# Performance work log

Measured on AMD Instinct MI355X. Metric: run time of the kernel, lower is better.

## Reference

```python
import jax, jax.numpy as jnp
import numpy as np
import math

B, T, C = 4, 1024, 768
H, K = 12, 10
D = C // H  # 64


def setup_inputs() -> dict:
    key = jax.random.key(0)
    ks = jax.random.split(key, 8)
    s = 1.0 / math.sqrt(C)
    return {
        "hidden_states": jax.random.normal(ks[0], (B, T, C), jnp.float32),
        "ucb_count_score": jax.random.uniform(ks[1], (B, H, T, T), jnp.float32),
        "Wq": jax.random.normal(ks[2], (C, C), jnp.float32) * s,
        "bq": jnp.zeros((C,), jnp.float32),
        "Wk": jax.random.normal(ks[3], (C, C), jnp.float32) * s,
        "bk": jnp.zeros((C,), jnp.float32),
        "Wv": jax.random.normal(ks[4], (C, C), jnp.float32) * s,
        "bv": jnp.zeros((C,), jnp.float32),
        "Wo": jax.random.normal(ks[5], (C, C), jnp.float32) * s,
        "bo": jnp.zeros((C,), jnp.float32),
        "counter": 2000,
        "ucb": 1,
    }


def _heads(x):
    # [B,T,C] -> [B,H,T,D]
    return x.reshape(B, T, H, D).transpose(0, 2, 1, 3)


def reference(hidden_states, ucb_count_score, Wq, bq, Wk, bk, Wv, bv, Wo, bo, counter, ucb):
    q = _heads(hidden_states @ Wq + bq)
    k = _heads(hidden_states @ Wk + bk)
    v = _heads(hidden_states @ Wv + bv)

    scores = jnp.einsum("bhqd,bhkd->bhqk", q, k) / math.sqrt(D)
    att = jax.nn.softmax(scores, axis=-1)

    if ucb and counter >= 1000:  # ucb_activation_step
        log_t = math.log(float(counter))
        ucb_scores = att + 1.0 * jnp.sqrt(log_t / (ucb_count_score + 1e-8))  # ucb_beta=1.0
        _, top_idx = jax.lax.top_k(ucb_scores, K)  # [B,H,T,K]
        # scatter 1.0 at top-k positions along last axis
        flat_idx = top_idx.reshape(-1, K)            # [N,K], N=B*H*T
        n = flat_idx.shape[0]
        mask = jnp.zeros((n, T), att.dtype).at[jnp.arange(n)[:, None], flat_idx].set(1.0)
        mask = mask.reshape(B, H, T, T)
        updated_count = ucb_count_score + mask
        sel = att * mask
        attention_probs = sel / (sel.sum(axis=-1, keepdims=True) + 1e-8)
    else:
        attention_probs = att
        updated_count = ucb_count_score

    ctx = jnp.einsum("bhqk,bhkd->bhqd", attention_probs, v)
    ctx = ctx.transpose(0, 2, 1, 3).reshape(B, T, C)
    out = ctx @ Wo + bo  # proj_dropout is identity in eval
    return out, attention_probs, updated_count
```

## Files before the change

### kernel.cpp

```cpp
#include <hip/hip_runtime.h>
#include <math.h>

namespace {

constexpr int Bc = 4, Tc = 1024, Cch = 768, Hc = 12, Dc = 64, KSEL = 10;
constexpr size_t BTC    = (size_t)Bc * Tc * Cch;
constexpr size_t PROBSN = (size_t)Bc * Hc * Tc * Tc;
constexpr size_t CC     = (size_t)Cch * Cch;

typedef __attribute__((ext_vector_type(8))) short          bf16x8;
typedef __attribute__((ext_vector_type(4))) float          f32x4;
typedef __attribute__((ext_vector_type(8))) unsigned short u16x8;

__device__ __forceinline__ unsigned short bf16rne(float x) {
  unsigned int u = __float_as_uint(x);
  return (unsigned short)((u + 0x7FFFu + ((u >> 16) & 1u)) >> 16);
}
__device__ __forceinline__ float bf16tof(unsigned short h) {
  return __uint_as_float(((unsigned int)h) << 16);
}

__device__ __forceinline__ void split8(const float4 v0, const float4 v1,
                                       u16x8& hh, u16x8& ll) {
  const float xs[8] = {v0.x, v0.y, v0.z, v0.w, v1.x, v1.y, v1.z, v1.w};
  #pragma unroll
  for (int e = 0; e < 8; ++e) {
    const unsigned short hb = bf16rne(xs[e]);
    hh[e] = hb;
    ll[e] = bf16rne(xs[e] - bf16tof(hb));
  }
}

template <int CTRL, int RM, bool BC>
__device__ __forceinline__ float dppmovf(float x, float oldv) {
  return __int_as_float(__builtin_amdgcn_update_dpp(
      __float_as_int(oldv), __float_as_int(x), CTRL, RM, 0xf, BC));
}

__device__ __forceinline__ float wave_fmax(float x) {
  x = fmaxf(x, dppmovf<0x111, 0xf, false>(x, x));
  x = fmaxf(x, dppmovf<0x112, 0xf, false>(x, x));
  x = fmaxf(x, dppmovf<0x114, 0xf, false>(x, x));
  x = fmaxf(x, dppmovf<0x118, 0xf, false>(x, x));
  x = fmaxf(x, dppmovf<0x142, 0xa, false>(x, x));
  x = fmaxf(x, dppmovf<0x143, 0xc, false>(x, x));
  return __int_as_float(__builtin_amdgcn_readlane(__float_as_int(x), 63));
}

__device__ __forceinline__ float wave_fsum(float x) {
  x += dppmovf<0x111, 0xf, true>(x, 0.f);
  x += dppmovf<0x112, 0xf, true>(x, 0.f);
  x += dppmovf<0x114, 0xf, true>(x, 0.f);
  x += dppmovf<0x118, 0xf, true>(x, 0.f);
  x += dppmovf<0x142, 0xa, true>(x, 0.f);
  x += dppmovf<0x143, 0xc, true>(x, 0.f);
  return __int_as_float(__builtin_amdgcn_readlane(__float_as_int(x), 63));
}

template <int CTRL, int RM>
__device__ __forceinline__ unsigned long long dppmax64_step(unsigned long long k) {
  const int lo = (int)(unsigned)(k & 0xFFFFFFFFull);
  const int hi = (int)(unsigned)(k >> 32);
  const int lo2 = __builtin_amdgcn_update_dpp(lo, lo, CTRL, RM, 0xf, false);
  const int hi2 = __builtin_amdgcn_update_dpp(hi, hi, CTRL, RM, 0xf, false);
  const unsigned long long k2 =
      ((unsigned long long)(unsigned)hi2 << 32) | (unsigned)lo2;
  return (k2 > k) ? k2 : k;
}

__device__ __forceinline__ unsigned long long wave_kmax(unsigned long long k) {
  k = dppmax64_step<0x111, 0xf>(k);
  k = dppmax64_step<0x112, 0xf>(k);
  k = dppmax64_step<0x114, 0xf>(k);
  k = dppmax64_step<0x118, 0xf>(k);
  k = dppmax64_step<0x142, 0xa>(k);
  k = dppmax64_step<0x143, 0xc>(k);
  const int lo = __builtin_amdgcn_readlane((int)(unsigned)(k & 0xFFFFFFFFull), 63);
  const int hi = __builtin_amdgcn_readlane((int)(unsigned)(k >> 32), 63);
  return ((unsigned long long)(unsigned)hi << 32) | (unsigned)lo;
}

__device__ __forceinline__ void splitT_body(
    const float* __restrict__ W,
    unsigned short* __restrict__ th, unsigned short* __restrict__ tl)
{
  __shared__ float tile[32][33];
  const int n0 = blockIdx.x * 32, k0 = blockIdx.y * 32;
  const int x = threadIdx.x & 31, y = threadIdx.x >> 5;

  #pragma unroll
  for (int i = 0; i < 4; ++i) {
    const int kk = y * 4 + i;
    tile[kk][x] = W[(size_t)(k0 + kk) * Cch + n0 + x];
  }
  __syncthreads();
  #pragma unroll
  for (int i = 0; i < 4; ++i) {
    const int nn = y * 4 + i;
    const float v = tile[x][nn];
    const unsigned short hb = bf16rne(v);
    th[(size_t)(n0 + nn) * Cch + k0 + x] = hb;
    tl[(size_t)(n0 + nn) * Cch + k0 + x] = bf16rne(v - bf16tof(hb));
  }
}

__global__ __launch_bounds__(256) void splitT_w(
    const float* __restrict__ W,
    unsigned short* __restrict__ th, unsigned short* __restrict__ tl)
{
  splitT_body(W, th, tl);
}

__global__ __launch_bounds__(256) void splitT_w3(
    const float* __restrict__ W0, const float* __restrict__ W1,
    const float* __restrict__ W2,
    unsigned short* __restrict__ th0, unsigned short* __restrict__ tl0,
    unsigned short* __restrict__ th1, unsigned short* __restrict__ tl1,
    unsigned short* __restrict__ th2, unsigned short* __restrict__ tl2)
{
  const int z = blockIdx.z;
  const float* W = (z == 0) ? W0 : (z == 1) ? W1 : W2;
  unsigned short* th = (z == 0) ? th0 : (z == 1) ? th1 : th2;
  unsigned short* tl = (z == 0) ? tl0 : (z == 1) ? tl1 : tl2;
  splitT_body(W, th, tl);
}

__global__ __launch_bounds__(256) void qkv_mfma(
    const float* __restrict__ hid,
    const unsigned short* __restrict__ wqth, const unsigned short* __restrict__ wqtl,
    const unsigned short* __restrict__ wkth, const unsigned short* __restrict__ wktl,
    const unsigned short* __restrict__ wvth, const unsigned short* __restrict__ wvtl,
    const float* __restrict__ bq, const float* __restrict__ bk,
    const float* __restrict__ bv,
    unsigned short* __restrict__ qh, unsigned short* __restrict__ ql,
    unsigned short* __restrict__ kh, unsigned short* __restrict__ kl,
    float* __restrict__ V)
{
  const int z = blockIdx.z;
  const unsigned short* __restrict__ Bhp = (z == 0) ? wqth : (z == 1) ? wkth : wvth;
  const unsigned short* __restrict__ Blp = (z == 0) ? wqtl : (z == 1) ? wktl : wvtl;
  const float* __restrict__ bias = (z == 0) ? bq : (z == 1) ? bk : bv;

  const int m0 = blockIdx.y * 64;
  const int n0 = blockIdx.x * 128;

  __shared__ unsigned short Ah[64][72],  Al[64][72];
  __shared__ unsigned short Bh[128][72], Bl[128][72];

  const int t    = threadIdx.x;
  const int lane = t & 63;
  const int wv   = t >> 6;
  const int wq   = (wv >> 1) * 32;
  const int wk   = (wv & 1) * 64;
  const int fr   = lane & 15;
  const int fg   = lane >> 4;

  f32x4 acc[2][4] = {};

  for (int k0 = 0; k0 < Cch; k0 += 64) {
    __syncthreads();
    #pragma unroll
    for (int i = 0; i < 2; ++i) {
      const int id = t + 256*i;
      const int r = id >> 3, c8 = (id & 7) * 8;
      const float4 v0 = *(const float4*)&hid[(size_t)(m0 + r)*Cch + k0 + c8];
      const float4 v1 = *(const float4*)&hid[(size_t)(m0 + r)*Cch + k0 + c8 + 4];
      u16x8 hh, ll;
      split8(v0, v1, hh, ll);
      *(u16x8*)&Ah[r][c8] = hh;
      *(u16x8*)&Al[r][c8] = ll;
    }
    #pragma unroll
    for (int i = 0; i < 4; ++i) {
      const int id = t + 256*i;
      const int r = id >> 3, c8 = (id & 7) * 8;
      *(u16x8*)&Bh[r][c8] = *(const u16x8*)&Bhp[(size_t)(n0 + r)*Cch + k0 + c8];
      *(u16x8*)&Bl[r][c8] = *(const u16x8*)&Blp[(size_t)(n0 + r)*Cch + k0 + c8];
    }
    __syncthreads();

    #pragma unroll
    for (int g2 = 0; g2 < 2; ++g2) {
      const int dof = g2*32 + 8*fg;
      bf16x8 aH[2], aL[2];
      #pragma unroll
      for (int qt = 0; qt < 2; ++qt) {
        aH[qt] = *(const bf16x8*)&Ah[wq + qt*16 + fr][dof];
        aL[qt] = *(const bf16x8*)&Al[wq + qt*16 + fr][dof];
      }
      #pragma unroll
      for (int kt = 0; kt < 4; ++kt) {
        const bf16x8 bH = *(const bf16x8*)&Bh[wk + kt*16 + fr][dof];
        const bf16x8 bL = *(const bf16x8*)&Bl[wk + kt*16 + fr][dof];
        #pragma unroll
        for (int qt = 0; qt < 2; ++qt) {
          acc[qt][kt] = __builtin_amdgcn_mfma_f32_16x16x32_bf16(
              aH[qt], bH, acc[qt][kt], 0, 0, 0);
          acc[qt][kt] = __builtin_amdgcn_mfma_f32_16x16x32_bf16(
              aH[qt], bL, acc[qt][kt], 0, 0, 0);
          acc[qt][kt] = __builtin_amdgcn_mfma_f32_16x16x32_bf16(
              aL[qt], bH, acc[qt][kt], 0, 0, 0);
        }
      }
    }
  }

  float bcol[4];
  #pragma unroll
  for (int kt = 0; kt < 4; ++kt) bcol[kt] = bias[n0 + wk + kt*16 + fr];

  unsigned short* __restrict__ dh = (z == 0) ? qh : kh;
  unsigned short* __restrict__ dl = (z == 0) ? ql : kl;

  #pragma unroll
  for (int qt = 0; qt < 2; ++qt) {
    #pragma unroll
    for (int j = 0; j < 4; ++j) {
      const int m  = m0 + wq + qt*16 + 4*fg + j;
      const int b  = m >> 10, tt = m & 1023;
      #pragma unroll
      for (int kt = 0; kt < 4; ++kt) {
        const int col = n0 + wk + kt*16 + fr;
        const float val = acc[qt][kt][j] + bcol[kt];
        const size_t idx =
            (((size_t)(b*Hc + (col >> 6)))*Tc + tt)*Dc + (col & 63);
        if (z < 2) {
          const unsigned short hb = bf16rne(val);
          dh[idx] = hb;
          dl[idx] = bf16rne(val - bf16tof(hb));
        } else {
          V[idx] = val;
        }
      }
    }
  }
}

__global__ __launch_bounds__(256) void score_mfma(
    const unsigned short* __restrict__ qhp, const unsigned short* __restrict__ qlp,
    const unsigned short* __restrict__ khp, const unsigned short* __restrict__ klp,
    float* __restrict__ scores)
{
  const int q0 = blockIdx.x * 64;
  const int bh = blockIdx.y;

  __shared__ unsigned short Qh[64][72],  Ql[64][72];
  __shared__ unsigned short Kh[128][72], Kl[128][72];

  const int t = threadIdx.x;
  const size_t qb = ((size_t)bh*Tc + q0) * Dc;

  #pragma unroll
  for (int i = 0; i < 2; ++i) {
    const int id = t + 256*i;
    const int r = id >> 3, c8 = (id & 7) * 8;
    *(u16x8*)&Qh[r][c8] = *(const u16x8*)&qhp[qb + (size_t)r*Dc + c8];
    *(u16x8*)&Ql[r][c8] = *(const u16x8*)&qlp[qb + (size_t)r*Dc + c8];
  }

  const int lane = t & 63;
  const int wv   = t >> 6;
  const int wq   = (wv >> 1) * 32;
  const int wk   = (wv & 1) * 64;
  const int fr   = lane & 15;
  const int fg   = lane >> 4;

  #pragma unroll 1
  for (int kc = 0; kc < 8; ++kc) {
    const int k0 = kc * 128;
    const size_t kb = ((size_t)bh*Tc + k0) * Dc;
    __syncthreads();
    #pragma unroll
    for (int i = 0; i < 4; ++i) {
      const int id = t + 256*i;
      const int r = id >> 3, c8 = (id & 7) * 8;
      *(u16x8*)&Kh[r][c8] = *(const u16x8*)&khp[kb + (size_t)r*Dc + c8];
      *(u16x8*)&Kl[r][c8] = *(const u16x8*)&klp[kb + (size_t)r*Dc + c8];
    }
    __syncthreads();

    f32x4 acc[2][4] = {};
    #pragma unroll
    for (int g2 = 0; g2 < 2; ++g2) {
      const int dof = g2*32 + 8*fg;
      bf16x8 aH[2], aL[2];
      #pragma unroll
      for (int qt = 0; qt < 2; ++qt) {
        aH[qt] = *(const bf16x8*)&Qh[wq + qt*16 + fr][dof];
        aL[qt] = *(const bf16x8*)&Ql[wq + qt*16 + fr][dof];
      }
      #pragma unroll
      for (int kt = 0; kt < 4; ++kt) {
        const bf16x8 bH = *(const bf16x8*)&Kh[wk + kt*16 + fr][dof];
        const bf16x8 bL = *(const bf16x8*)&Kl[wk + kt*16 + fr][dof];
        #pragma unroll
        for (int qt = 0; qt < 2; ++qt) {
          acc[qt][kt] = __builtin_amdgcn_mfma_f32_16x16x32_bf16(
              aH[qt], bH, acc[qt][kt], 0, 0, 0);
          acc[qt][kt] = __builtin_amdgcn_mfma_f32_16x16x32_bf16(
              aH[qt], bL, acc[qt][kt], 0, 0, 0);
          acc[qt][kt] = __builtin_amdgcn_mfma_f32_16x16x32_bf16(
              aL[qt], bH, acc[qt][kt], 0, 0, 0);
        }
      }
    }

    #pragma unroll
    for (int qt = 0; qt < 2; ++qt) {
      #pragma unroll
      for (int j = 0; j < 4; ++j) {
        const int qrow = q0 + wq + qt*16 + 4*fg + j;
        const size_t rb = ((size_t)bh * Tc + qrow) * Tc + k0 + wk;
        #pragma unroll
        for (int kt = 0; kt < 4; ++kt)
          scores[rb + kt*16 + fr] = acc[qt][kt][j] * 0.125f;
      }
    }
  }
}

__global__ __launch_bounds__(256, 4) void ucb_topk(
    const float* __restrict__ qkv,
    const float* __restrict__ count_in,
    const int*   __restrict__ counter_p,
    const int*   __restrict__ ucb_p,
    float* __restrict__ probs,
    float* __restrict__ count_out,
    float* __restrict__ ctx)
{
  const int bh   = blockIdx.y;
  const int lane = threadIdx.x & 63;
  const int wv   = threadIdx.x >> 6;
  const int row  = blockIdx.x * 4 + wv;
  const int b = bh / Hc, h = bh % Hc;
  const size_t rb = ((size_t)bh * Tc + row) * Tc;
  const float* __restrict__ Vh = qkv + 2*BTC + (size_t)bh * Tc * Dc;

  __shared__ float psel[4][KSEL];

  const int  counter = counter_p[0];
  const int  ucbf    = ucb_p[0];
  const bool do_ucb  = (ucbf != 0) && (counter >= 1000);
  const float lt     = do_ucb ? logf((float)counter) : 0.f;

  float s[16];
  #pragma unroll
  for (int w = 0; w < 16; ++w) s[w] = probs[rb + lane + 64*w];

  float mx = -INFINITY;
  #pragma unroll
  for (int w = 0; w < 16; ++w) mx = fmaxf(mx, s[w]);
  mx = wave_fmax(mx);

  float sum = 0.f;
  #pragma unroll
  for (int w = 0; w < 16; ++w) { s[w] = __expf(s[w] - mx); sum += s[w]; }
  sum = wave_fsum(sum);

  const float rsum = 1.0f / sum;
  #pragma unroll
  for (int w = 0; w < 16; ++w) s[w] = s[w] * rsum;

  if (do_ucb) {
    const float sqlt = sqrtf(lt);

    unsigned long long key[16];
    #pragma unroll
    for (int w = 0; w < 16; ++w) {
      const float c = count_in[rb + lane + 64*w];
      count_out[rb + lane + 64*w] = c;
      const float u = fmaf(sqlt, rsqrtf(c + 1e-8f), s[w]);
      key[w] = ((unsigned long long)__float_as_uint(u) << 32)
             | (unsigned long long)(~(unsigned)(lane + (w << 6)));
    }

    unsigned selmask = 0u;
    unsigned long long rpack = 0ull;
    int ks[KSEL];

    #pragma unroll
    for (int r = 0; r < KSEL; ++r) {
      unsigned long long t0[8];
      #pragma unroll
      for (int w = 0; w < 8; ++w) {
        const unsigned long long a =
            ((selmask >> (2*w)) & 1u) ? 0ull : key[2*w];
        const unsigned long long bb =
            ((selmask >> (2*w + 1)) & 1u) ? 0ull : key[2*w + 1];
        t0[w] = (a > bb) ? a : bb;
      }
      unsigned long long t1[4];
      #pragma unroll
      for (int w = 0; w < 4; ++w)
        t1[w] = (t0[2*w] > t0[2*w+1]) ? t0[2*w] : t0[2*w+1];
      unsigned long long t2a = (t1[0] > t1[1]) ? t1[0] : t1[1];
      unsigned long long t2b = (t1[2] > t1[3]) ? t1[2] : t1[3];
      unsigned long long m   = (t2a > t2b) ? t2a : t2b;

      m = wave_kmax(m);

      const int idx = (int)(~(unsigned)(m & 0xFFFFFFFFull));
      ks[r] = idx;
      if ((idx & 63) == lane) {
        const int wsel = idx >> 6;
        selmask |= 1u << wsel;
        rpack   |= ((unsigned long long)r) << (4 * wsel);
      }
    }

    #pragma unroll
    for (int w = 0; w < 16; ++w) {
      if ((selmask >> w) & 1u) {
        const int r = (int)((rpack >> (4 * w)) & 15ull);
        psel[wv][r] = s[w];
      }
    }
    __syncthreads();

    float pvv[KSEL];
    float denom = 1e-8f;
    #pragma unroll
    for (int r = 0; r < KSEL; ++r) { pvv[r] = psel[wv][r]; denom += pvv[r]; }
    const float rden = 1.0f / denom;

    #pragma unroll
    for (int w = 0; w < 16; ++w) {
      const bool sb = (selmask >> w) & 1u;
      probs[rb + lane + 64*w] = sb ? (s[w] * rden) : 0.0f;
    }
    #pragma unroll
    for (int r = 0; r < KSEL; ++r) {
      if ((ks[r] & 63) == lane)
        count_out[rb + ks[r]] = count_in[rb + ks[r]] + 1.0f;
    }

    float cd = 0.f;
    #pragma unroll
    for (int r = 0; r < KSEL; ++r)
      cd += pvv[r] * Vh[(size_t)ks[r] * Dc + lane];
    ctx[((size_t)b*Tc + row)*Cch + h*Dc + lane] = cd * rden;
  } else {
    #pragma unroll
    for (int w = 0; w < 16; ++w) {
      probs[rb + lane + 64*w]     = s[w];
      count_out[rb + lane + 64*w] = count_in[rb + lane + 64*w];
    }
  }
}

__global__ __launch_bounds__(256) void pv_gemm(
    const float* __restrict__ probs,
    const float* __restrict__ Vm,
    float* __restrict__ ctx,
    const int* __restrict__ counter_p,
    const int* __restrict__ ucb_p)
{
  if ((ucb_p[0] != 0) && (counter_p[0] >= 1000)) return;

  const int bh = blockIdx.y;
  const int q0 = blockIdx.x * 64;
  const int b = bh / Hc, h = bh % Hc;

  __shared__ float aT[32][68];
  __shared__ float vN[32][68];

  const int t  = threadIdx.x;
  const int tn = t & 15;
  const int tq = t >> 4;

  float acc[4][4];
  #pragma unroll
  for (int i = 0; i < 4; ++i)
    #pragma unroll
    for (int j = 0; j < 4; ++j) acc[i][j] = 0.f;

  for (int k0 = 0; k0 < Tc; k0 += 32) {
    __syncthreads();
    #pragma unroll
    for (int p = 0; p < 2; ++p) {
      const int id = t + 256*p;
      const int r = id >> 3, c = id & 7;
      const float4 v =
          *(const float4*)&probs[((size_t)bh*Tc + q0 + r)*Tc + k0 + 4*c];
      aT[4*c + 0][r] = v.x; aT[4*c + 1][r] = v.y;
      aT[4*c + 2][r] = v.z; aT[4*c + 3][r] = v.w;
    }
    #pragma unroll
    for (int p = 0; p < 2; ++p) {
      const int id = t + 256*p;
      const int kk = id >> 4, dcc = id & 15;
      const float4 v = *(const float4*)&Vm[((size_t)bh*Tc + k0 + kk)*Dc + 4*dcc];
      *(float4*)&vN[kk][4*dcc] = v;
    }
    __syncthreads();
    #pragma unroll
    for (int kk = 0; kk < 32; ++kk) {
      const float4 a  = *(const float4*)&aT[kk][4*tq];
      const float4 vv = *(const float4*)&vN[kk][4*tn];
      const float av[4] = {a.x, a.y, a.z, a.w};
      const float bw[4] = {vv.x, vv.y, vv.z, vv.w};
      #pragma unroll
      for (int qi = 0; qi < 4; ++qi)
        #pragma unroll
        for (int ni = 0; ni < 4; ++ni) acc[qi][ni] += av[qi] * bw[ni];
    }
  }

  #pragma unroll
  for (int qi = 0; qi < 4; ++qi) {
    const int tt = q0 + 4*tq + qi;
    float4 o;
    o.x = acc[qi][0]; o.y = acc[qi][1]; o.z = acc[qi][2]; o.w = acc[qi][3];
    *(float4*)&ctx[((size_t)b*Tc + tt)*Cch + h*Dc + 4*tn] = o;
  }
}

__global__ __launch_bounds__(256) void out_mfma(
    const float* __restrict__ ctx,
    const unsigned short* __restrict__ bth, const unsigned short* __restrict__ btl,
    const float* __restrict__ bias,
    float* __restrict__ out)
{
  const int m0 = blockIdx.y * 64;
  const int n0 = blockIdx.x * 128;

  __shared__ unsigned short Ah[64][72],  Al[64][72];
  __shared__ unsigned short Bh[128][72], Bl[128][72];

  const int t    = threadIdx.x;
  const int lane = t & 63;
  const int wv   = t >> 6;
  const int wq   = (wv >> 1) * 32;
  const int wk   = (wv & 1) * 64;
  const int fr   = lane & 15;
  const int fg   = lane >> 4;

  f32x4 acc[2][4] = {};

  for (int k0 = 0; k0 < Cch; k0 += 64) {
    __syncthreads();
    #pragma unroll
    for (int i = 0; i < 2; ++i) {
      const int id = t + 256*i;
      const int r = id >> 3, c8 = (id & 7) * 8;
      const float4 v0 = *(const float4*)&ctx[(size_t)(m0 + r)*Cch + k0 + c8];
      const float4 v1 = *(const float4*)&ctx[(size_t)(m0 + r)*Cch + k0 + c8 + 4];
      u16x8 hh, ll;
      split8(v0, v1, hh, ll);
      *(u16x8*)&Ah[r][c8] = hh;
      *(u16x8*)&Al[r][c8] = ll;
    }
    #pragma unroll
    for (int i = 0; i < 4; ++i) {
      const int id = t + 256*i;
      const int r = id >> 3, c8 = (id & 7) * 8;
      *(u16x8*)&Bh[r][c8] = *(const u16x8*)&bth[(size_t)(n0 + r)*Cch + k0 + c8];
      *(u16x8*)&Bl[r][c8] = *(const u16x8*)&btl[(size_t)(n0 + r)*Cch + k0 + c8];
    }
    __syncthreads();

    #pragma unroll
    for (int g2 = 0; g2 < 2; ++g2) {
      const int dof = g2*32 + 8*fg;
      bf16x8 aH[2], aL[2];
      #pragma unroll
      for (int qt = 0; qt < 2; ++qt) {
        aH[qt] = *(const bf16x8*)&Ah[wq + qt*16 + fr][dof];
        aL[qt] = *(const bf16x8*)&Al[wq + qt*16 + fr][dof];
      }
      #pragma unroll
      for (int kt = 0; kt < 4; ++kt) {
        const bf16x8 bH = *(const bf16x8*)&Bh[wk + kt*16 + fr][dof];
        const bf16x8 bL = *(const bf16x8*)&Bl[wk + kt*16 + fr][dof];
        #pragma unroll
        for (int qt = 0; qt < 2; ++qt) {
          acc[qt][kt] = __builtin_amdgcn_mfma_f32_16x16x32_bf16(
              aH[qt], bH, acc[qt][kt], 0, 0, 0);
          acc[qt][kt] = __builtin_amdgcn_mfma_f32_16x16x32_bf16(
              aH[qt], bL, acc[qt][kt], 0, 0, 0);
          acc[qt][kt] = __builtin_amdgcn_mfma_f32_16x16x32_bf16(
              aL[qt], bH, acc[qt][kt], 0, 0, 0);
        }
      }
    }
  }

  float bcol[4];
  #pragma unroll
  for (int kt = 0; kt < 4; ++kt) bcol[kt] = bias[n0 + wk + kt*16 + fr];

  #pragma unroll
  for (int qt = 0; qt < 2; ++qt) {
    #pragma unroll
    for (int j = 0; j < 4; ++j) {
      const int m = m0 + wq + qt*16 + 4*fg + j;
      #pragma unroll
      for (int kt = 0; kt < 4; ++kt) {
        const int col = n0 + wk + kt*16 + fr;
        out[(size_t)m * Cch + col] = acc[qt][kt][j] + bcol[kt];
      }
    }
  }
}

}

extern "C" void kernel_launch(void* const* d_in, const int* in_sizes, int n_in,
                              void* d_out, int out_size, void* d_ws, size_t ws_size,
                              hipStream_t stream) {
  (void)in_sizes; (void)n_in; (void)out_size; (void)ws_size;

  const float* hid  = (const float*)d_in[0];
  const float* cnt  = (const float*)d_in[1];
  const float* Wq   = (const float*)d_in[2];
  const float* bq   = (const float*)d_in[3];
  const float* Wk   = (const float*)d_in[4];
  const float* bk   = (const float*)d_in[5];
  const float* Wv   = (const float*)d_in[6];
  const float* bv   = (const float*)d_in[7];
  const float* Wo   = (const float*)d_in[8];
  const float* bo   = (const float*)d_in[9];
  const int* counter = (const int*)d_in[10];
  const int* ucb     = (const int*)d_in[11];

  float* out       = (float*)d_out;
  float* probs     = out + BTC;
  float* count_out = probs + PROBSN;

  float* ws  = (float*)d_ws;
  float* V   = ws + 2*BTC;
  float* ctx = ws + 3*BTC;
  unsigned short* qkb = (unsigned short*)d_ws;
  unsigned short* qh = qkb;
  unsigned short* ql = qkb + BTC;
  unsigned short* kh = qkb + 2*BTC;
  unsigned short* kl = qkb + 3*BTC;

  unsigned short* cvt  = (unsigned short*)count_out;
  unsigned short* wqth = cvt;
  unsigned short* wqtl = wqth + CC;
  unsigned short* wkth = wqtl + CC;
  unsigned short* wktl = wkth + CC;
  unsigned short* wvth = wktl + CC;
  unsigned short* wvtl = wvth + CC;

  unsigned short* woth = qkb;
  unsigned short* wotl = qkb + CC;

  splitT_w3<<<dim3(24, 24, 3), 256, 0, stream>>>(
      Wq, Wk, Wv, wqth, wqtl, wkth, wktl, wvth, wvtl);

  qkv_mfma<<<dim3(Cch/128, (Bc*Tc)/64, 3), 256, 0, stream>>>(
      hid, wqth, wqtl, wkth, wktl, wvth, wvtl,
      bq, bk, bv, qh, ql, kh, kl, V);

  score_mfma<<<dim3(Tc/64, Bc*Hc), 256, 0, stream>>>(
      qh, ql, kh, kl, probs);

  splitT_w<<<dim3(24, 24), 256, 0, stream>>>(Wo, woth, wotl);

  ucb_topk<<<dim3(Tc/4, Bc*Hc), 256, 0, stream>>>(
      ws, cnt, counter, ucb, probs, count_out, ctx);

  pv_gemm<<<dim3(Tc/64, Bc*Hc), 256, 0, stream>>>(
      probs, V, ctx, counter, ucb);

  out_mfma<<<dim3(Cch/128, (Bc*Tc)/64), 256, 0, stream>>>(
      ctx, woth, wotl, bo, out);
}
```

Before: 371.6 us.

## Fuse QK score computation into softmax/UCB top-k kernel

Merges the score GEMM and the softmax/UCB top-k kernel. Each 1024-thread block computes QK^T scores for 16 query rows through LDS and keeps them in registers, so the full fp32 score matrix is no longer written to and re-read from global memory. The cost is that every block reloads all of K for only 16 query rows. Each wave also does just one 16x16 MFMA tile per chunk, with a large LDS footprint and lower occupancy.

```diff
diff --git a/kernel.cpp b/kernel.cpp
--- a/kernel.cpp
+++ b/kernel.cpp
@@ -236,90 +236,9 @@
   }
 }
 
-__global__ __launch_bounds__(256) void score_mfma(
+__global__ __launch_bounds__(1024, 4) void score_topk(
     const unsigned short* __restrict__ qhp, const unsigned short* __restrict__ qlp,
     const unsigned short* __restrict__ khp, const unsigned short* __restrict__ klp,
-    float* __restrict__ scores)
-{
-  const int q0 = blockIdx.x * 64;
-  const int bh = blockIdx.y;
-
-  __shared__ unsigned short Qh[64][72],  Ql[64][72];
-  __shared__ unsigned short Kh[128][72], Kl[128][72];
-
-  const int t = threadIdx.x;
-  const size_t qb = ((size_t)bh*Tc + q0) * Dc;
-
-  #pragma unroll
-  for (int i = 0; i < 2; ++i) {
-    const int id = t + 256*i;
-    const int r = id >> 3, c8 = (id & 7) * 8;
-    *(u16x8*)&Qh[r][c8] = *(const u16x8*)&qhp[qb + (size_t)r*Dc + c8];
-    *(u16x8*)&Ql[r][c8] = *(const u16x8*)&qlp[qb + (size_t)r*Dc + c8];
-  }
-
-  const int lane = t & 63;
-  const int wv   = t >> 6;
-  const int wq   = (wv >> 1) * 32;
-  const int wk   = (wv & 1) * 64;
-  const int fr   = lane & 15;
-  const int fg   = lane >> 4;
-
-  #pragma unroll 1
-  for (int kc = 0; kc < 8; ++kc) {
-    const int k0 = kc * 128;
-    const size_t kb = ((size_t)bh*Tc + k0) * Dc;
-    __syncthreads();
-    #pragma unroll
-    for (int i = 0; i < 4; ++i) {
-      const int id = t + 256*i;
-      const int r = id >> 3, c8 = (id & 7) * 8;
-      *(u16x8*)&Kh[r][c8] = *(const u16x8*)&khp[kb + (size_t)r*Dc + c8];
-      *(u16x8*)&Kl[r][c8] = *(const u16x8*)&klp[kb + (size_t)r*Dc + c8];
-    }
-    __syncthreads();
-
-    f32x4 acc[2][4] = {};
-    #pragma unroll
-    for (int g2 = 0; g2 < 2; ++g2) {
-      const int dof = g2*32 + 8*fg;
-      bf16x8 aH[2], aL[2];
-      #pragma unroll
-      for (int qt = 0; qt < 2; ++qt) {
-        aH[qt] = *(const bf16x8*)&Qh[wq + qt*16 + fr][dof];
-        aL[qt] = *(const bf16x8*)&Ql[wq + qt*16 + fr][dof];
-      }
-      #pragma unroll
-      for (int kt = 0; kt < 4; ++kt) {
-        const bf16x8 bH = *(const bf16x8*)&Kh[wk + kt*16 + fr][dof];
-        const bf16x8 bL = *(const bf16x8*)&Kl[wk + kt*16 + fr][dof];
-        #pragma unroll
-        for (int qt = 0; qt < 2; ++qt) {
-          acc[qt][kt] = __builtin_amdgcn_mfma_f32_16x16x32_bf16(
-              aH[qt], bH, acc[qt][kt], 0, 0, 0);
-          acc[qt][kt] = __builtin_amdgcn_mfma_f32_16x16x32_bf16(
-              aH[qt], bL, acc[qt][kt], 0, 0, 0);
-          acc[qt][kt] = __builtin_amdgcn_mfma_f32_16x16x32_bf16(
-              aL[qt], bH, acc[qt][kt], 0, 0, 0);
-        }
-      }
-    }
-
-    #pragma unroll
-    for (int qt = 0; qt < 2; ++qt) {
-      #pragma unroll
-      for (int j = 0; j < 4; ++j) {
-        const int qrow = q0 + wq + qt*16 + 4*fg + j;
-        const size_t rb = ((size_t)bh * Tc + qrow) * Tc + k0 + wk;
-        #pragma unroll
-        for (int kt = 0; kt < 4; ++kt)
-          scores[rb + kt*16 + fr] = acc[qt][kt][j] * 0.125f;
-      }
-    }
-  }
-}
-
-__global__ __launch_bounds__(256, 4) void ucb_topk(
     const float* __restrict__ qkv,
     const float* __restrict__ count_in,
     const int*   __restrict__ counter_p,
@@ -328,24 +247,78 @@
     float* __restrict__ count_out,
     float* __restrict__ ctx)
 {
-  const int bh   = blockIdx.y;
-  const int lane = threadIdx.x & 63;
-  const int wv   = threadIdx.x >> 6;
-  const int row  = blockIdx.x * 4 + wv;
-  const int b = bh / Hc, h = bh % Hc;
+  const int bh = blockIdx.y;
+  const int q0 = blockIdx.x * 16;
+  const int b  = bh / Hc, h = bh % Hc;
+
+  __shared__ unsigned short Qh[16][72],  Ql[16][72];
+  __shared__ unsigned short Kh[256][72], Kl[256][72];
+  __shared__ float sc[16][260];
+  __shared__ float psel[16][KSEL];
+
+  const int t    = threadIdx.x;
+  const int lane = t & 63;
+  const int wv   = t >> 6;
+  const int fr   = lane & 15;
+  const int fg   = lane >> 4;
+
+  {
+    const size_t qb = ((size_t)bh*Tc + q0) * Dc;
+    if (t < 128) {
+      const int r = t >> 3, c8 = (t & 7) * 8;
+      *(u16x8*)&Qh[r][c8] = *(const u16x8*)&qhp[qb + (size_t)r*Dc + c8];
+    } else if (t < 256) {
+      const int t2 = t - 128;
+      const int r = t2 >> 3, c8 = (t2 & 7) * 8;
+      *(u16x8*)&Ql[r][c8] = *(const u16x8*)&qlp[qb + (size_t)r*Dc + c8];
+    }
+  }
+
+  float s[16];
+  #pragma unroll
+  for (int kc = 0; kc < 4; ++kc) {
+    {
+      const size_t kb = ((size_t)bh*Tc + kc*256) * Dc;
+      #pragma unroll
+      for (int i = 0; i < 2; ++i) {
+        const int id = t + 1024*i;
+        const int r = id >> 3, c8 = (id & 7) * 8;
+        *(u16x8*)&Kh[r][c8] = *(const u16x8*)&khp[kb + (size_t)r*Dc + c8];
+        *(u16x8*)&Kl[r][c8] = *(const u16x8*)&klp[kb + (size_t)r*Dc + c8];
+      }
+    }
+    __syncthreads();
+
+    f32x4 acc = {};
+    #pragma unroll
+    for (int g2 = 0; g2 < 2; ++g2) {
+      const int dof = g2*32 + 8*fg;
+      const bf16x8 aH = *(const bf16x8*)&Qh[fr][dof];
+      const bf16x8 aL = *(const bf16x8*)&Ql[fr][dof];
+      const bf16x8 bH = *(const bf16x8*)&Kh[wv*16 + fr][dof];
+      const bf16x8 bL = *(const bf16x8*)&Kl[wv*16 + fr][dof];
+      acc = __builtin_amdgcn_mfma_f32_16x16x32_bf16(aH, bH, acc, 0, 0, 0);
+      acc = __builtin_amdgcn_mfma_f32_16x16x32_bf16(aH, bL, acc, 0, 0, 0);
+      acc = __builtin_amdgcn_mfma_f32_16x16x32_bf16(aL, bH, acc, 0, 0, 0);
+    }
+    #pragma unroll
+    for (int j = 0; j < 4; ++j)
+      sc[4*fg + j][wv*16 + fr] = acc[j];
+    __syncthreads();
+
+    #pragma unroll
+    for (int p = 0; p < 4; ++p)
+      s[4*kc + p] = sc[wv][64*p + lane] * 0.125f;
+  }
+
+  const int row = q0 + wv;
   const size_t rb = ((size_t)bh * Tc + row) * Tc;
   const float* __restrict__ Vh = qkv + 2*BTC + (size_t)bh * Tc * Dc;
-
-  __shared__ float psel[4][KSEL];
 
   const int  counter = counter_p[0];
   const int  ucbf    = ucb_p[0];
   const bool do_ucb  = (ucbf != 0) && (counter >= 1000);
   const float lt     = do_ucb ? logf((float)counter) : 0.f;
-
-  float s[16];
-  #pragma unroll
-  for (int w = 0; w < 16; ++w) s[w] = probs[rb + lane + 64*w];
 
   float mx = -INFINITY;
   #pragma unroll
@@ -654,13 +627,10 @@
       hid, wqth, wqtl, wkth, wktl, wvth, wvtl,
       bq, bk, bv, qh, ql, kh, kl, V);
 
-  score_mfma<<<dim3(Tc/64, Bc*Hc), 256, 0, stream>>>(
-      qh, ql, kh, kl, probs);
+  score_topk<<<dim3(Tc/16, Bc*Hc), 1024, 0, stream>>>(
+      qh, ql, kh, kl, ws, cnt, counter, ucb, probs, count_out, ctx);
 
   splitT_w<<<dim3(24, 24), 256, 0, stream>>>(Wo, woth, wotl);
-
-  ucb_topk<<<dim3(Tc/4, Bc*Hc), 256, 0, stream>>>(
-      ws, cnt, counter, ucb, probs, count_out, ctx);
 
   pv_gemm<<<dim3(Tc/64, Bc*Hc), 256, 0, stream>>>(
       probs, V, ctx, counter, ucb);
```

New measurement: 454.8 us, median of 2. 1.22x slower.
